# Kernel tuning notes

Hardware: AMD Instinct MI355X
Metric: run time of the kernel (lower is better)

The kernel has to match this reference:

```python
import jax, jax.numpy as jnp
import numpy as np

LEAKY_ALPHA = 0.2  # TF default for tf.nn.leaky_relu

def setup_inputs() -> dict:
    key = jax.random.key(0)
    k1, k2, k3 = jax.random.split(key, 3)
    B, N, D = 8192, 2048, 128
    patient_features = jax.random.normal(k1, (B, D), dtype=jnp.float32)
    disease_nodes = jax.random.normal(k2, (N, D), dtype=jnp.float32)
    attn_kernel = jax.random.normal(k3, (2 * D, 1), dtype=jnp.float32)
    return {"patient_features": patient_features,
            "disease_nodes": disease_nodes,
            "attn_kernel": attn_kernel}

def reference(patient_features, disease_nodes, attn_kernel):
    # patient_features: [B, D]; disease_nodes: [N, D]; attn_kernel: [2D, 1]
    D = patient_features.shape[-1]
    a_p = attn_kernel[:D, 0]   # [D] acts on the patient half of the concat
    a_n = attn_kernel[D:, 0]   # [D] acts on the disease-node half
    # concat([p, n]) @ a  ==  p @ a_p  +  n @ a_n  (exact decomposition)
    scores = (patient_features @ a_p)[:, None] + (disease_nodes @ a_n)[None, :]  # [B, N]
    attn_weights = jax.nn.softmax(jax.nn.leaky_relu(scores, LEAKY_ALPHA), axis=1)  # [B, N]
    node_influence = attn_weights @ disease_nodes  # [B, D]
    return patient_features + node_influence
```

## Files before the change

kernel.cpp:

```cpp
#include <hip/hip_runtime.h>
#include <hip/hip_bf16.h>

#define LEAKY 0.2f
#define B_TOT 8192
#define N_TOT 2048
#define D_TOT 128
#define BM 32

typedef float f32x4 __attribute__((ext_vector_type(4)));
typedef short bf16x8 __attribute__((ext_vector_type(8)));
typedef unsigned short u16x8 __attribute__((ext_vector_type(8)));

static __device__ __forceinline__ unsigned short f2bf(float x) {
    return __builtin_bit_cast(unsigned short, __float2bfloat16(x));
}


__global__ __launch_bounds__(256) void prep_kernel(const float* __restrict__ disease,
                                                   const float* __restrict__ ak,
                                                   float* __restrict__ q,
                                                   uint4* __restrict__ DnTf) {
    __shared__ float tile[32][129];
    __shared__ float a_s[D_TOT];
    const int tid = threadIdx.x;
    const int b = blockIdx.x;
    const int r0 = b * 32;

    if (tid < D_TOT) a_s[tid] = ak[D_TOT + tid];
    #pragma unroll
    for (int t = 0; t < 4; ++t) {
        int idx = tid + t * 256;
        int row = idx >> 5;
        int cv = (idx & 31) * 4;
        float4 v = *(const float4*)(disease + (size_t)(r0 + row) * D_TOT + cv);
        tile[row][cv] = v.x; tile[row][cv + 1] = v.y;
        tile[row][cv + 2] = v.z; tile[row][cv + 3] = v.w;
    }
    __syncthreads();

    const int wave = tid >> 6, lane = tid & 63;
    #pragma unroll
    for (int rr = 0; rr < 8; ++rr) {
        int r = wave * 8 + rr;
        float s = tile[r][lane] * a_s[lane] + tile[r][lane + 64] * a_s[lane + 64];
        #pragma unroll
        for (int off = 32; off; off >>= 1) s += __shfl_xor(s, off);
        if (lane == 0) q[r0 + r] = s;
    }

    #pragma unroll
    for (int h = 0; h < 2; ++h) {
        const int c  = tid + h * 256;
        const int kg = c >> 7;
        const int col = c & 127;
        const int ct = col >> 4, cl = col & 15;
        unsigned u[4];
        #pragma unroll
        for (int jj = 0; jj < 4; ++jj) {
            unsigned lo = f2bf(tile[kg * 8 + 2 * jj][col]);
            unsigned hi = f2bf(tile[kg * 8 + 2 * jj + 1][col]);
            u[jj] = lo | (hi << 16);
        }
        DnTf[((size_t)b * 8 + ct) * 64 + kg * 16 + cl] = make_uint4(u[0], u[1], u[2], u[3]);
    }
}

__global__ __launch_bounds__(1024, 4) void gat_mfma(const float* __restrict__ patient,
                                                    const float* __restrict__ ak,
                                                    const float* __restrict__ q,
                                                    const unsigned short* __restrict__ DnTb,
                                                    float* __restrict__ out) {
    __shared__ __align__(16) float eq1_s[N_TOT];
    __shared__ __align__(16) float eq2_s[N_TOT];
    __shared__ float red_s[3][2][2][1024];
    __shared__ float a_s[D_TOT];
    __shared__ float p_s[BM], E1_s[BM], E2_s[BM], T1_s[BM], S_s[BM];
    __shared__ float red16[16];

    const int tid  = threadIdx.x;
    const int wave = tid >> 6;
    const int lane = tid & 63;
    const int b0   = blockIdx.x * BM;

    if (tid < D_TOT) a_s[tid] = ak[tid];
    __syncthreads();

    float mx = -1e30f;
    for (int i = tid; i < N_TOT; i += 1024) {
        float qq = q[i];
        eq1_s[i] = __expf(qq);
        eq2_s[i] = __expf(LEAKY * qq);
        mx = fmaxf(mx, qq);
    }
    #pragma unroll
    for (int off = 32; off; off >>= 1) mx = fmaxf(mx, __shfl_xor(mx, off));
    if (lane == 0) red16[wave] = mx;

    #pragma unroll
    for (int rr = 0; rr < 2; ++rr) {
        const int row = wave * 2 + rr;
        const float* pr = patient + (size_t)(b0 + row) * D_TOT;
        float s = pr[lane] * a_s[lane] + pr[lane + 64] * a_s[lane + 64];
        #pragma unroll
        for (int off = 32; off; off >>= 1) s += __shfl_xor(s, off);
        if (lane == 0) p_s[row] = s;
    }
    __syncthreads();

    float qmax = red16[0];
    #pragma unroll
    for (int i = 1; i < 16; ++i) qmax = fmaxf(qmax, red16[i]);

    if (tid < BM) {
        const float pv = p_s[tid];
        const float xm = pv + qmax;
        const float m = fmaxf(xm, LEAKY * xm);
        E1_s[tid] = __expf(pv - m);
        E2_s[tid] = __expf(LEAKY * pv - m);
        T1_s[tid] = __expf(-pv);
    }
    __syncthreads();

    #pragma unroll
    for (int rr = 0; rr < 2; ++rr) {
        const int row = wave * 2 + rr;
        const float T1 = T1_s[row];
        float s1 = 0.f, s2 = 0.f;
        for (int n = lane; n < N_TOT; n += 64) {
            float e1 = eq1_s[n], e2 = eq2_s[n];
            bool c = e1 > T1;
            s1 += c ? e1 : 0.f;
            s2 += c ? 0.f : e2;
        }
        #pragma unroll
        for (int off = 32; off; off >>= 1) {
            s1 += __shfl_xor(s1, off);
            s2 += __shfl_xor(s2, off);
        }
        if (lane == 0) S_s[row] = E1_s[row] * s1 + E2_s[row] * s2;
    }
    __syncthreads();

    const int cl = lane & 15;
    const int kg = lane >> 4;
    const int cw = wave & 1;
    const int rt = (wave >> 1) & 1;
    const int kq = wave >> 2;
    const int arow = rt * 16 + cl;

    const float E1A = E1_s[arow], E2A = E2_s[arow], T1A = T1_s[arow];

    f32x4 acc[4] = {};

    #pragma unroll 4
    for (int kt = kq * 16; kt < kq * 16 + 16; ++kt) {
        const int gk = kt * 32 + kg * 8;
        const float4 e1a = *(const float4*)&eq1_s[gk];
        const float4 e1b = *(const float4*)&eq1_s[gk + 4];
        const float4 e2a = *(const float4*)&eq2_s[gk];
        const float4 e2b = *(const float4*)&eq2_s[gk + 4];
        bf16x8 bf[4];
        #pragma unroll
        for (int t = 0; t < 4; ++t)
            bf[t] = *(const bf16x8*)(DnTb + (((size_t)kt * 8 + cw * 4 + t) * 64 + lane) * 8);

        const float e1v[8] = {e1a.x, e1a.y, e1a.z, e1a.w, e1b.x, e1b.y, e1b.z, e1b.w};
        const float e2v[8] = {e2a.x, e2a.y, e2a.z, e2a.w, e2b.x, e2b.y, e2b.z, e2b.w};
        u16x8 aw;
        #pragma unroll
        for (int j = 0; j < 8; ++j) {
            bool c = e1v[j] > T1A;
            float w = (c ? E1A : E2A) * (c ? e1v[j] : e2v[j]);
            aw[j] = f2bf(w);
        }
        const bf16x8 a0 = __builtin_bit_cast(bf16x8, aw);

        acc[0] = __builtin_amdgcn_mfma_f32_16x16x32_bf16(a0, bf[0], acc[0], 0, 0, 0);
        acc[1] = __builtin_amdgcn_mfma_f32_16x16x32_bf16(a0, bf[1], acc[1], 0, 0, 0);
        acc[2] = __builtin_amdgcn_mfma_f32_16x16x32_bf16(a0, bf[2], acc[2], 0, 0, 0);
        acc[3] = __builtin_amdgcn_mfma_f32_16x16x32_bf16(a0, bf[3], acc[3], 0, 0, 0);
    }

    __syncthreads();
    if (kq > 0) {
        float* rb = &red_s[kq - 1][rt][cw][0];
        #pragma unroll
        for (int t = 0; t < 4; ++t)
            #pragma unroll
            for (int i = 0; i < 4; ++i)
                rb[t * 256 + (kg * 4 + i) * 16 + cl] = acc[t][i];
    }
    __syncthreads();
    if (kq == 0) {
        #pragma unroll
        for (int t = 0; t < 4; ++t)
            #pragma unroll
            for (int i = 0; i < 4; ++i) {
                const int idx = t * 256 + (kg * 4 + i) * 16 + cl;
                acc[t][i] += red_s[0][rt][cw][idx] + red_s[1][rt][cw][idx]
                           + red_s[2][rt][cw][idx];
            }
        float inv[4];
        #pragma unroll
        for (int i = 0; i < 4; ++i) inv[i] = 1.0f / S_s[rt * 16 + kg * 4 + i];
        #pragma unroll
        for (int t = 0; t < 4; ++t)
            #pragma unroll
            for (int i = 0; i < 4; ++i) {
                const int row = b0 + rt * 16 + kg * 4 + i;
                const int col = cw * 64 + t * 16 + cl;
                out[(size_t)row * D_TOT + col] =
                    patient[(size_t)row * D_TOT + col] + acc[t][i] * inv[i];
            }
    }
}


__global__ __launch_bounds__(256) void pq_fb(const float* __restrict__ patient,
                                             const float* __restrict__ disease,
                                             const float* __restrict__ ak,
                                             float* __restrict__ p,
                                             float* __restrict__ q) {
    int gid  = blockIdx.x * blockDim.x + threadIdx.x;
    int wid  = gid >> 6;
    int lane = gid & 63;
    const float* src;
    const float* a;
    float* dst;
    if (wid < B_TOT) {
        src = patient + (size_t)wid * D_TOT; a = ak; dst = p + wid;
    } else {
        src = disease + (size_t)(wid - B_TOT) * D_TOT; a = ak + D_TOT; dst = q + (wid - B_TOT);
    }
    float s = src[lane] * a[lane] + src[lane + 64] * a[lane + 64];
    #pragma unroll
    for (int off = 32; off; off >>= 1) s += __shfl_xor(s, off);
    if (lane == 0) *dst = s;
}

#define FBP 16
#define FNT 256
__global__ __launch_bounds__(256) void gat_fb(const float* __restrict__ patient,
                                              const float* __restrict__ disease,
                                              const float* __restrict__ p,
                                              const float* __restrict__ q,
                                              float* __restrict__ out) {
    __shared__ float q_s[N_TOT];
    __shared__ float w_s[FBP][FNT];
    __shared__ float m_s[FBP], S_s[FBP], pp_s[FBP];
    const int tid = threadIdx.x;
    const int b0  = blockIdx.x * FBP;
    for (int i = tid; i < N_TOT; i += 256) q_s[i] = q[i];
    if (tid < FBP) pp_s[tid] = p[b0 + tid];
    __syncthreads();
    const int wave = tid >> 6, lane = tid & 63;
    for (int pi = wave * 4; pi < wave * 4 + 4; ++pi) {
        float pp = pp_s[pi];
        float mx = -1e30f;
        for (int n = lane; n < N_TOT; n += 64) {
            float x = pp + q_s[n]; x = x > 0.0f ? x : LEAKY * x; mx = fmaxf(mx, x);
        }
        #pragma unroll
        for (int off = 32; off; off >>= 1) mx = fmaxf(mx, __shfl_xor(mx, off));
        float sum = 0.0f;
        for (int n = lane; n < N_TOT; n += 64) {
            float x = pp + q_s[n]; x = x > 0.0f ? x : LEAKY * x; sum += __expf(x - mx);
        }
        #pragma unroll
        for (int off = 32; off; off >>= 1) sum += __shfl_xor(sum, off);
        if (lane == 0) { m_s[pi] = mx; S_s[pi] = sum; }
    }
    __syncthreads();
    const int d2 = tid & 31;
    const int pg = tid >> 5;
    const int p0 = 2 * pg, p1 = 2 * pg + 1;
    float4 acc0 = make_float4(0.f, 0.f, 0.f, 0.f);
    float4 acc1 = make_float4(0.f, 0.f, 0.f, 0.f);
    for (int n0 = 0; n0 < N_TOT; n0 += FNT) {
        __syncthreads();
        for (int i = tid; i < FBP * FNT; i += 256) {
            int pi = i >> 8;
            int nt = i & (FNT - 1);
            float x = pp_s[pi] + q_s[n0 + nt];
            x = x > 0.0f ? x : LEAKY * x;
            w_s[pi][nt] = __expf(x - m_s[pi]);
        }
        __syncthreads();
        const float* drow = disease + (size_t)n0 * D_TOT + d2 * 4;
        #pragma unroll 4
        for (int nt = 0; nt < FNT; ++nt) {
            float4 dv = *reinterpret_cast<const float4*>(drow + (size_t)nt * D_TOT);
            float w0 = w_s[p0][nt];
            float w1 = w_s[p1][nt];
            acc0.x += w0 * dv.x; acc0.y += w0 * dv.y; acc0.z += w0 * dv.z; acc0.w += w0 * dv.w;
            acc1.x += w1 * dv.x; acc1.y += w1 * dv.y; acc1.z += w1 * dv.z; acc1.w += w1 * dv.w;
        }
    }
    const float inv0 = 1.0f / S_s[p0];
    const float inv1 = 1.0f / S_s[p1];
    {
        size_t off = (size_t)(b0 + p0) * D_TOT + d2 * 4;
        float4 pf = *reinterpret_cast<const float4*>(patient + off);
        float4 o;
        o.x = pf.x + acc0.x * inv0; o.y = pf.y + acc0.y * inv0;
        o.z = pf.z + acc0.z * inv0; o.w = pf.w + acc0.w * inv0;
        *reinterpret_cast<float4*>(reinterpret_cast<float*>(out) + off) = o;
    }
    {
        size_t off = (size_t)(b0 + p1) * D_TOT + d2 * 4;
        float4 pf = *reinterpret_cast<const float4*>(patient + off);
        float4 o;
        o.x = pf.x + acc1.x * inv1; o.y = pf.y + acc1.y * inv1;
        o.z = pf.z + acc1.z * inv1; o.w = pf.w + acc1.w * inv1;
        *reinterpret_cast<float4*>(reinterpret_cast<float*>(out) + off) = o;
    }
}

extern "C" void kernel_launch(void* const* d_in, const int* in_sizes, int n_in,
                              void* d_out, int out_size, void* d_ws, size_t ws_size,
                              hipStream_t stream) {
    const float* patient = (const float*)d_in[0];
    const float* disease = (const float*)d_in[1];
    const float* ak      = (const float*)d_in[2];
    float* out = (float*)d_out;

    const size_t need_fast = (size_t)512 * 1024 + 8192;
    if (ws_size >= need_fast) {
        uint4* DnTf = (uint4*)d_ws;
        float* q    = (float*)((char*)d_ws + 512 * 1024);
        prep_kernel<<<N_TOT / 32, 256, 0, stream>>>(disease, ak, q, DnTf);
        gat_mfma<<<B_TOT / BM, 1024, 0, stream>>>(patient, ak, q,
                                                  (const unsigned short*)DnTf, out);
    } else {
        float* p = (float*)d_ws;
        float* q = p + B_TOT;
        pq_fb<<<(B_TOT + N_TOT) / 4, 256, 0, stream>>>(patient, disease, ak, p, q);
        gat_fb<<<B_TOT / FBP, 256, 0, stream>>>(patient, disease, p, q, out);
    }
}
```

Measured before the change: 27.72 us.

## Halve rows per block, split K eight ways, replace threshold select with fmax

Each block now handles 16 patient rows instead of 32. Its 16 waves split the N reduction into 8 K-chunks instead of 4, and the partials are reduced through a larger shared buffer. The leaky-relu softmax weight is now computed as fmax(E1*e1, E2*e2) rather than a threshold compare and select, which removes the T1 exp and the per-row T1 table. The aim is twice as many blocks for better CU occupancy and fewer ALU ops per weight. The cost is more per-block overhead (recomputing the exp tables, more reduction traffic) and twice as many DnTb reads in total.

```diff
diff --git a/kernel.cpp b/kernel.cpp
--- a/kernel.cpp
+++ b/kernel.cpp
@@ -5,7 +5,7 @@
 #define B_TOT 8192
 #define N_TOT 2048
 #define D_TOT 128
-#define BM 32
+#define BM 16
 
 typedef float f32x4 __attribute__((ext_vector_type(4)));
 typedef short bf16x8 __attribute__((ext_vector_type(8)));
@@ -65,16 +65,16 @@
     }
 }
 
-__global__ __launch_bounds__(1024, 4) void gat_mfma(const float* __restrict__ patient,
+__global__ __launch_bounds__(1024, 8) void gat_mfma(const float* __restrict__ patient,
                                                     const float* __restrict__ ak,
                                                     const float* __restrict__ q,
                                                     const unsigned short* __restrict__ DnTb,
                                                     float* __restrict__ out) {
     __shared__ __align__(16) float eq1_s[N_TOT];
     __shared__ __align__(16) float eq2_s[N_TOT];
-    __shared__ float red_s[3][2][2][1024];
+    __shared__ float red_s[7][2][1024];
     __shared__ float a_s[D_TOT];
-    __shared__ float p_s[BM], E1_s[BM], E2_s[BM], T1_s[BM], S_s[BM];
+    __shared__ float p_s[BM], E1_s[BM], E2_s[BM], S_s[BM];
     __shared__ float red16[16];
 
     const int tid  = threadIdx.x;
@@ -96,64 +96,49 @@
     for (int off = 32; off; off >>= 1) mx = fmaxf(mx, __shfl_xor(mx, off));
     if (lane == 0) red16[wave] = mx;
 
-    #pragma unroll
-    for (int rr = 0; rr < 2; ++rr) {
-        const int row = wave * 2 + rr;
-        const float* pr = patient + (size_t)(b0 + row) * D_TOT;
+    {
+        const float* pr = patient + (size_t)(b0 + wave) * D_TOT;
         float s = pr[lane] * a_s[lane] + pr[lane + 64] * a_s[lane + 64];
         #pragma unroll
         for (int off = 32; off; off >>= 1) s += __shfl_xor(s, off);
-        if (lane == 0) p_s[row] = s;
-    }
-    __syncthreads();
-
-    float qmax = red16[0];
-    #pragma unroll
-    for (int i = 1; i < 16; ++i) qmax = fmaxf(qmax, red16[i]);
+        if (lane == 0) p_s[wave] = s;
+    }
+    __syncthreads();
 
     if (tid < BM) {
+        float qmax = red16[0];
+        #pragma unroll
+        for (int i = 1; i < 16; ++i) qmax = fmaxf(qmax, red16[i]);
         const float pv = p_s[tid];
         const float xm = pv + qmax;
         const float m = fmaxf(xm, LEAKY * xm);
         E1_s[tid] = __expf(pv - m);
         E2_s[tid] = __expf(LEAKY * pv - m);
-        T1_s[tid] = __expf(-pv);
-    }
-    __syncthreads();
-
-    #pragma unroll
-    for (int rr = 0; rr < 2; ++rr) {
-        const int row = wave * 2 + rr;
-        const float T1 = T1_s[row];
-        float s1 = 0.f, s2 = 0.f;
-        for (int n = lane; n < N_TOT; n += 64) {
-            float e1 = eq1_s[n], e2 = eq2_s[n];
-            bool c = e1 > T1;
-            s1 += c ? e1 : 0.f;
-            s2 += c ? 0.f : e2;
-        }
-        #pragma unroll
-        for (int off = 32; off; off >>= 1) {
-            s1 += __shfl_xor(s1, off);
-            s2 += __shfl_xor(s2, off);
-        }
-        if (lane == 0) S_s[row] = E1_s[row] * s1 + E2_s[row] * s2;
+    }
+    __syncthreads();
+
+    {
+        const float E1 = E1_s[wave], E2 = E2_s[wave];
+        float s = 0.f;
+        for (int n = lane; n < N_TOT; n += 64)
+            s += fmaxf(E1 * eq1_s[n], E2 * eq2_s[n]);
+        #pragma unroll
+        for (int off = 32; off; off >>= 1) s += __shfl_xor(s, off);
+        if (lane == 0) S_s[wave] = s;
     }
     __syncthreads();
 
     const int cl = lane & 15;
     const int kg = lane >> 4;
     const int cw = wave & 1;
-    const int rt = (wave >> 1) & 1;
-    const int kq = wave >> 2;
-    const int arow = rt * 16 + cl;
-
-    const float E1A = E1_s[arow], E2A = E2_s[arow], T1A = T1_s[arow];
+    const int kq = wave >> 1;
+
+    const float E1A = E1_s[cl], E2A = E2_s[cl];
 
     f32x4 acc[4] = {};
 
-    #pragma unroll 4
-    for (int kt = kq * 16; kt < kq * 16 + 16; ++kt) {
+    #pragma unroll 2
+    for (int kt = kq * 8; kt < kq * 8 + 8; ++kt) {
         const int gk = kt * 32 + kg * 8;
         const float4 e1a = *(const float4*)&eq1_s[gk];
         const float4 e1b = *(const float4*)&eq1_s[gk + 4];
@@ -168,11 +153,8 @@
         const float e2v[8] = {e2a.x, e2a.y, e2a.z, e2a.w, e2b.x, e2b.y, e2b.z, e2b.w};
         u16x8 aw;
         #pragma unroll
-        for (int j = 0; j < 8; ++j) {
-            bool c = e1v[j] > T1A;
-            float w = (c ? E1A : E2A) * (c ? e1v[j] : e2v[j]);
-            aw[j] = f2bf(w);
-        }
+        for (int j = 0; j < 8; ++j)
+            aw[j] = f2bf(fmaxf(E1A * e1v[j], E2A * e2v[j]));
         const bf16x8 a0 = __builtin_bit_cast(bf16x8, aw);
 
         acc[0] = __builtin_amdgcn_mfma_f32_16x16x32_bf16(a0, bf[0], acc[0], 0, 0, 0);
@@ -183,7 +165,7 @@
 
     __syncthreads();
     if (kq > 0) {
-        float* rb = &red_s[kq - 1][rt][cw][0];
+        float* rb = &red_s[kq - 1][cw][0];
         #pragma unroll
         for (int t = 0; t < 4; ++t)
             #pragma unroll
@@ -197,17 +179,19 @@
             #pragma unroll
             for (int i = 0; i < 4; ++i) {
                 const int idx = t * 256 + (kg * 4 + i) * 16 + cl;
-                acc[t][i] += red_s[0][rt][cw][idx] + red_s[1][rt][cw][idx]
-                           + red_s[2][rt][cw][idx];
+                float s = acc[t][i];
+                #pragma unroll
+                for (int j = 0; j < 7; ++j) s += red_s[j][cw][idx];
+                acc[t][i] = s;
             }
         float inv[4];
         #pragma unroll
-        for (int i = 0; i < 4; ++i) inv[i] = 1.0f / S_s[rt * 16 + kg * 4 + i];
+        for (int i = 0; i < 4; ++i) inv[i] = 1.0f / S_s[kg * 4 + i];
         #pragma unroll
         for (int t = 0; t < 4; ++t)
             #pragma unroll
             for (int i = 0; i < 4; ++i) {
-                const int row = b0 + rt * 16 + kg * 4 + i;
+                const int row = b0 + kg * 4 + i;
                 const int col = cw * 64 + t * 16 + cl;
                 out[(size_t)row * D_TOT + col] =
                     patient[(size_t)row * D_TOT + col] + acc[t][i] * inv[i];
```

New measurement: 29.07 us. 1.05x slower.
